# Optimization experiments

Hardware: AMD Instinct MI355X
Metric: run time of the kernel (lower is better)

The kernel has to match this reference:

```python
import jax, jax.numpy as jnp
import numpy as np

N = 100000   # total nodes in batched graph
E = 600000   # total edges
B = 64       # graphs in batch
H = 128      # hidden_dim
A = 64       # action_dim
L = 4        # num mpnn layers
LOG_STD_MIN, LOG_STD_MAX = -20.0, 2.0


def setup_inputs() -> dict:
    key = jax.random.key(0)
    ks = jax.random.split(key, 40)
    s = 0.05

    def w(k, shape):
        return (jax.random.normal(k, shape, jnp.float32) * s)

    inp = {}
    inp["node_feat"] = jax.random.normal(ks[0], (N, 7), jnp.float32)
    inp["edge_feat"] = jax.random.normal(ks[1], (E, 2), jnp.float32)
    # node encoder: Linear(7,H) -> ReLU -> Linear(H,H)
    inp["ne_w1"] = w(ks[2], (7, H)); inp["ne_b1"] = jnp.zeros((H,), jnp.float32)
    inp["ne_w2"] = w(ks[3], (H, H)); inp["ne_b2"] = jnp.zeros((H,), jnp.float32)
    # edge encoder: Linear(2,H) -> ReLU -> Linear(H,H)
    inp["ee_w1"] = w(ks[4], (2, H)); inp["ee_b1"] = jnp.zeros((H,), jnp.float32)
    inp["ee_w2"] = w(ks[5], (H, H)); inp["ee_b2"] = jnp.zeros((H,), jnp.float32)
    # per-layer message net: Linear(3H,H) -> ReLU -> Linear(H,H)  (stacked over L)
    inp["msg_w1"] = w(ks[6], (L, 3 * H, H)); inp["msg_b1"] = jnp.zeros((L, H), jnp.float32)
    inp["msg_w2"] = w(ks[7], (L, H, H));     inp["msg_b2"] = jnp.zeros((L, H), jnp.float32)
    # per-layer update net: Linear(2H,H) -> ReLU -> Linear(H,H)
    inp["upd_w1"] = w(ks[8], (L, 2 * H, H)); inp["upd_b1"] = jnp.zeros((L, H), jnp.float32)
    inp["upd_w2"] = w(ks[9], (L, H, H));     inp["upd_b2"] = jnp.zeros((L, H), jnp.float32)
    # attention-pooling gate: Linear(H,H) -> ReLU -> Linear(H,1)
    inp["gate_w1"] = w(ks[10], (H, H)); inp["gate_b1"] = jnp.zeros((H,), jnp.float32)
    inp["gate_w2"] = w(ks[11], (H, 1)); inp["gate_b2"] = jnp.zeros((1,), jnp.float32)
    # policy net: Linear(H,H) -> ReLU -> Linear(H,H) -> ReLU -> Linear(H,2A)
    inp["pol_w1"] = w(ks[12], (H, H));     inp["pol_b1"] = jnp.zeros((H,), jnp.float32)
    inp["pol_w2"] = w(ks[13], (H, H));     inp["pol_b2"] = jnp.zeros((H,), jnp.float32)
    inp["pol_w3"] = w(ks[14], (H, 2 * A)); inp["pol_b3"] = jnp.zeros((2 * A,), jnp.float32)
    # graph connectivity
    inp["src"] = jax.random.randint(ks[15], (E,), 0, N)
    inp["dst"] = jax.random.randint(ks[16], (E,), 0, N)
    inp["graph_id"] = jnp.sort(jax.random.randint(ks[17], (N,), 0, B))
    return inp


def _mlp2(x, w1, b1, w2, b2):
    return jax.nn.relu(x @ w1 + b1) @ w2 + b2


def reference(node_feat, edge_feat,
              ne_w1, ne_b1, ne_w2, ne_b2,
              ee_w1, ee_b1, ee_w2, ee_b2,
              msg_w1, msg_b1, msg_w2, msg_b2,
              upd_w1, upd_b1, upd_w2, upd_b2,
              gate_w1, gate_b1, gate_w2, gate_b2,
              pol_w1, pol_b1, pol_w2, pol_b2, pol_w3, pol_b3,
              src, dst, graph_id):
    # encode
    h = _mlp2(node_feat, ne_w1, ne_b1, ne_w2, ne_b2)          # [N, H]
    e = _mlp2(edge_feat, ee_w1, ee_b1, ee_w2, ee_b2)          # [E, H]
    # MPNN layers with residual (h = layer(h) + h)
    for l in range(L):
        msg_in = jnp.concatenate([h[src], h[dst], e], axis=1)  # [E, 3H]
        m = _mlp2(msg_in, msg_w1[l], msg_b1[l], msg_w2[l], msg_b2[l])  # [E, H]
        h_agg = jax.ops.segment_sum(m, dst, num_segments=N)    # [N, H]
        upd_in = jnp.concatenate([h, h_agg], axis=1)           # [N, 2H]
        h = _mlp2(upd_in, upd_w1[l], upd_b1[l], upd_w2[l], upd_b2[l]) + h
    # global attention pooling (per-graph segment softmax over gate logits)
    gate = _mlp2(h, gate_w1, gate_b1, gate_w2, gate_b2)[:, 0]  # [N]
    gmax = jax.ops.segment_max(gate, graph_id, num_segments=B)  # [B]
    ex = jnp.exp(gate - gmax[graph_id])                        # [N]
    z = jax.ops.segment_sum(ex, graph_id, num_segments=B)      # [B]
    alpha = ex / z[graph_id]                                   # [N]
    emb = jax.ops.segment_sum(alpha[:, None] * h, graph_id, num_segments=B)  # [B, H]
    # policy head
    out = jax.nn.relu(jax.nn.relu(emb @ pol_w1 + pol_b1) @ pol_w2 + pol_b2) @ pol_w3 + pol_b3  # [B, 2A]
    mean, log_std = out[:, :A], out[:, A:]
    log_std = jnp.clip(log_std, LOG_STD_MIN, LOG_STD_MAX)
    std = jnp.exp(log_std)
    return (mean, std)
```

## Files before the change

### kernel.cpp

```cpp
#include <hip/hip_runtime.h>
#include <stdint.h>

#define NN 100000
#define NE 600000
#define NG 64
#define HD 128
#define HD2 (HD*HD)
#define NLAYER 4
#define SCAN_NB 391
#define NTILES ((NN + 63) / 64)
#define PSLICE 16

typedef unsigned short u16;
typedef unsigned int u32;
typedef unsigned long long u64;
typedef __attribute__((ext_vector_type(8))) short bf16x8;
typedef __attribute__((ext_vector_type(4))) float f32x4;

__device__ __forceinline__ float bf2f(u32 v) { return __uint_as_float(v << 16); }
__device__ __forceinline__ u16 f2bf(float f) {
    u32 u = __float_as_uint(f);
    return (u16)((u + 0x7FFFu + ((u >> 16) & 1u)) >> 16);
}
__device__ __forceinline__ u32 pk2(float a, float b) {
    return (u32)f2bf(a) | ((u32)f2bf(b) << 16);
}

template<bool RELU, bool GATE>
__global__ __launch_bounds__(256, 3) void mgemm_kernel(
    const u16* __restrict__ Xb, const u16* __restrict__ Wt,
    const float* __restrict__ bias, const float* __restrict__ degscale,
    const u16* __restrict__ addend, u16* __restrict__ out, int M,
    const float* __restrict__ gw2, const float* __restrict__ gb2,
    float* __restrict__ gate)
{
    __shared__ u16 WsL[HD * HD];
    __shared__ u16 XsL[64 * HD];
    const int t = threadIdx.x;
    const int lane = t & 63, wave = t >> 6;
    const int cj = ((lane >> 4) << 2);

    for (int i = t; i < HD * 16; i += 256) {
        const int row = i >> 4, c16 = i & 15;
        uint4 v = *(const uint4*)(Wt + (size_t)row * HD + c16 * 8);
        *(uint4*)((char*)WsL + (((row << 8) + (c16 << 4)) ^ ((row & 7) << 4))) = v;
    }
    float4 bcol[8];
    #pragma unroll
    for (int ct = 0; ct < 8; ct++)
        bcol[ct] = bias ? *(const float4*)(bias + ct * 16 + cj)
                        : make_float4(0.f, 0.f, 0.f, 0.f);
    float4 gwv[8];
    if (GATE) {
        #pragma unroll
        for (int ct = 0; ct < 8; ct++)
            gwv[ct] = *(const float4*)(gw2 + ct * 16 + cj);
    }

    const int arow = wave * 16 + (lane & 15);
    const int alin = (arow << 8) + ((lane >> 4) << 4);
    const int axor = (arow & 7) << 4;
    __syncthreads();

    for (int tile = blockIdx.x; tile < NTILES; tile += gridDim.x) {
        const int r0 = tile << 6;
        for (int i = t; i < 64 * 16; i += 256) {
            const int row = i >> 4, c16 = i & 15;
            const int rg = r0 + row;
            uint4 v = make_uint4(0, 0, 0, 0);
            if (rg < M) v = *(const uint4*)(Xb + (size_t)rg * HD + c16 * 8);
            *(uint4*)((char*)XsL + (((row << 8) + (c16 << 4)) ^ ((row & 7) << 4))) = v;
        }
        __syncthreads();

        bf16x8 a[4];
        #pragma unroll
        for (int ks = 0; ks < 4; ks++)
            a[ks] = *(const bf16x8*)((const char*)XsL + ((alin + ks * 64) ^ axor));

        f32x4 acc[8];
        #pragma unroll
        for (int ct = 0; ct < 8; ct++) {
            acc[ct][0] = 0.f; acc[ct][1] = 0.f; acc[ct][2] = 0.f; acc[ct][3] = 0.f;
        }
        #pragma unroll
        for (int ct = 0; ct < 8; ct++) {
            const int bn = ct * 16 + (lane & 15);
            #pragma unroll
            for (int ks = 0; ks < 4; ks++) {
                bf16x8 breg = *(const bf16x8*)((const char*)WsL +
                    (((bn << 8) + ks * 64 + ((lane >> 4) << 4)) ^ ((bn & 7) << 4)));
                acc[ct] = __builtin_amdgcn_mfma_f32_16x16x32_bf16(breg, a[ks], acc[ct], 0, 0, 0);
            }
        }

        const int orow = r0 + wave * 16 + (lane & 15);
        const bool rv = orow < M;
        float gdot = 0.f;
        const float ds = (degscale && rv) ? degscale[orow] : 1.f;
        #pragma unroll
        for (int ct = 0; ct < 8; ct++) {
            const int c0 = ct * 16 + cj;
            float v0 = acc[ct][0], v1 = acc[ct][1], v2 = acc[ct][2], v3 = acc[ct][3];
            if (bias) {
                v0 += bcol[ct].x * ds; v1 += bcol[ct].y * ds;
                v2 += bcol[ct].z * ds; v3 += bcol[ct].w * ds;
            }
            if (addend && rv) {
                ushort4 av = *(const ushort4*)(addend + (size_t)orow * HD + c0);
                v0 += bf2f(av.x); v1 += bf2f(av.y); v2 += bf2f(av.z); v3 += bf2f(av.w);
            }
            if (RELU) {
                v0 = fmaxf(v0, 0.f); v1 = fmaxf(v1, 0.f);
                v2 = fmaxf(v2, 0.f); v3 = fmaxf(v3, 0.f);
            }
            if (GATE) {
                gdot += v0 * gwv[ct].x + v1 * gwv[ct].y + v2 * gwv[ct].z + v3 * gwv[ct].w;
            } else if (rv) {
                ushort4 pk;
                pk.x = f2bf(v0); pk.y = f2bf(v1); pk.z = f2bf(v2); pk.w = f2bf(v3);
                *(ushort4*)(out + (size_t)orow * HD + c0) = pk;
            }
        }
        if (GATE) {
            gdot += __shfl_xor(gdot, 16, 64);
            gdot += __shfl_xor(gdot, 32, 64);
            if ((lane >> 4) == 0 && rv) gate[orow] = gdot + gb2[0];
        }
        __syncthreads();
    }
}

__global__ __launch_bounds__(256, 2) void pqtgemm_kernel(
    const u16* __restrict__ Xb, const u16* __restrict__ WtP,
    const u16* __restrict__ WtQ, const u16* __restrict__ WtT,
    const float* __restrict__ tb, u16* __restrict__ outP,
    u16* __restrict__ outQ, u16* __restrict__ outT, int M)
{
    __shared__ u16 WsL[2 * HD * HD];
    __shared__ u16 XsL[64 * HD];
    const int t = threadIdx.x;
    const int lane = t & 63, wave = t >> 6;
    const int cj = ((lane >> 4) << 2);

    for (int i = t; i < 2 * HD * 16; i += 256) {
        const int w = i >> 11;
        const int j = i & 2047;
        const int row = j >> 4, c16 = j & 15;
        const u16* Wt = w ? WtQ : WtP;
        uint4 v = *(const uint4*)(Wt + (size_t)row * HD + c16 * 8);
        *(uint4*)((char*)WsL + w * 32768 +
                  (((row << 8) + (c16 << 4)) ^ ((row & 7) << 4))) = v;
    }
    bf16x8 treg[8][4];
    #pragma unroll
    for (int ct = 0; ct < 8; ct++) {
        const int bn = ct * 16 + (lane & 15);
        #pragma unroll
        for (int ks = 0; ks < 4; ks++)
            treg[ct][ks] = *(const bf16x8*)(WtT + (size_t)bn * HD + ks * 32 + ((lane >> 4) << 3));
    }
    float4 tbc[8];
    #pragma unroll
    for (int ct = 0; ct < 8; ct++)
        tbc[ct] = *(const float4*)(tb + ct * 16 + cj);

    const int arow = wave * 16 + (lane & 15);
    const int alin = (arow << 8) + ((lane >> 4) << 4);
    const int axor = (arow & 7) << 4;
    __syncthreads();

    for (int tile = blockIdx.x; tile < NTILES; tile += gridDim.x) {
        const int r0 = tile << 6;
        for (int i = t; i < 64 * 16; i += 256) {
            const int row = i >> 4, c16 = i & 15;
            const int rg = r0 + row;
            uint4 v = make_uint4(0, 0, 0, 0);
            if (rg < M) v = *(const uint4*)(Xb + (size_t)rg * HD + c16 * 8);
            *(uint4*)((char*)XsL + (((row << 8) + (c16 << 4)) ^ ((row & 7) << 4))) = v;
        }
        __syncthreads();

        bf16x8 a[4];
        #pragma unroll
        for (int ks = 0; ks < 4; ks++)
            a[ks] = *(const bf16x8*)((const char*)XsL + ((alin + ks * 64) ^ axor));

        const int orow = r0 + wave * 16 + (lane & 15);
        const bool rv = orow < M;

        #pragma unroll
        for (int o = 0; o < 2; o++) {
            f32x4 acc[8];
            #pragma unroll
            for (int ct = 0; ct < 8; ct++) {
                acc[ct][0] = 0.f; acc[ct][1] = 0.f; acc[ct][2] = 0.f; acc[ct][3] = 0.f;
            }
            #pragma unroll
            for (int ct = 0; ct < 8; ct++) {
                const int bn = ct * 16 + (lane & 15);
                #pragma unroll
                for (int ks = 0; ks < 4; ks++) {
                    bf16x8 breg = *(const bf16x8*)((const char*)WsL + o * 32768 +
                        (((bn << 8) + ks * 64 + ((lane >> 4) << 4)) ^ ((bn & 7) << 4)));
                    acc[ct] = __builtin_amdgcn_mfma_f32_16x16x32_bf16(breg, a[ks], acc[ct], 0, 0, 0);
                }
            }
            if (rv) {
                u16* out = o ? outQ : outP;
                #pragma unroll
                for (int ct = 0; ct < 8; ct++) {
                    ushort4 pk;
                    pk.x = f2bf(acc[ct][0]); pk.y = f2bf(acc[ct][1]);
                    pk.z = f2bf(acc[ct][2]); pk.w = f2bf(acc[ct][3]);
                    *(ushort4*)(out + (size_t)orow * HD + ct * 16 + cj) = pk;
                }
            }
        }
        {
            f32x4 acc[8];
            #pragma unroll
            for (int ct = 0; ct < 8; ct++) {
                acc[ct][0] = 0.f; acc[ct][1] = 0.f; acc[ct][2] = 0.f; acc[ct][3] = 0.f;
            }
            #pragma unroll
            for (int ct = 0; ct < 8; ct++)
                #pragma unroll
                for (int ks = 0; ks < 4; ks++)
                    acc[ct] = __builtin_amdgcn_mfma_f32_16x16x32_bf16(treg[ct][ks], a[ks], acc[ct], 0, 0, 0);
            if (rv) {
                #pragma unroll
                for (int ct = 0; ct < 8; ct++) {
                    ushort4 pk;
                    pk.x = f2bf(acc[ct][0] + tbc[ct].x);
                    pk.y = f2bf(acc[ct][1] + tbc[ct].y);
                    pk.z = f2bf(acc[ct][2] + tbc[ct].z);
                    pk.w = f2bf(acc[ct][3] + tbc[ct].w);
                    *(ushort4*)(outT + (size_t)orow * HD + ct * 16 + cj) = pk;
                }
            }
        }
        __syncthreads();
    }
}

__global__ __launch_bounds__(256, 2) void edge_mfma_kernel(
    const float2* __restrict__ sef, const int* __restrict__ ssrc,
    const int* __restrict__ sdst, const int* __restrict__ off,
    const float* __restrict__ ew1, const float* __restrict__ eb1,
    const u16* __restrict__ Mt, const float* __restrict__ mvec,
    const u16* __restrict__ P, const u16* __restrict__ Q,
    u16* __restrict__ agg)
{
    __shared__ __align__(16) char XHT[HD * 72 * 2];
    __shared__ u16 PsL[64 * 136];
    __shared__ u16 QsL[32 * 136];
    __shared__ u64 dlocL[8];
    __shared__ int nsrcL[2][64];
    __shared__ float ew1L[2 * HD];
    __shared__ float eb1L[HD];
    u16* HT = (u16*)XHT;
    const int t = threadIdx.x, lane = t & 63, wave = t >> 6;
    const int cj = (lane >> 4) << 2;
    const int n0 = blockIdx.x * 32;

    ew1L[t] = ew1[t];
    if (t < HD) eb1L[t] = eb1[t];
    for (int i = t; i < 32 * 32; i += 256) {
        const int row = i >> 5, c4 = (i & 31) * 4;
        *(ushort4*)(QsL + row * 136 + c4) = *(const ushort4*)(Q + (size_t)(n0 + row) * HD + c4);
    }

    float4 mvv[8];
    #pragma unroll
    for (int ct = 0; ct < 8; ct++) mvv[ct] = *(const float4*)(mvec + ct * 16 + cj);

    bf16x8 breg[8][4];
    #pragma unroll
    for (int ct = 0; ct < 8; ct++) {
        const int bn = ct * 16 + (lane & 15);
        #pragma unroll
        for (int ks = 0; ks < 4; ks++)
            breg[ct][ks] = *(const bf16x8*)(Mt + (size_t)bn * HD + ks * 32 + ((lane >> 4) << 3));
    }

    const int rt = wave & 1;
    const int c2b = (wave >> 1) * 4;
    const int nodeid = rt * 16 + (lane & 15);
    f32x4 acc2[4];
    #pragma unroll
    for (int i = 0; i < 4; i++) {
        acc2[i][0] = 0.f; acc2[i][1] = 0.f; acc2[i][2] = 0.f; acc2[i][3] = 0.f;
    }

    const int e0 = off[n0], e1 = off[n0 + 32];
    const int arow = wave * 16 + (lane & 15);
    const int alin = (arow << 8) + ((lane >> 4) << 4);
    const int axor = (arow & 7) << 4;
    const int el = wave * 16 + (lane & 15);
    if (t < 64) nsrcL[0][t] = (e0 + t < e1) ? ssrc[e0 + t] : 0;
    __syncthreads();

    int buf = 0;
    for (int base = e0; base < e1; base += 64) {
        for (int i = t; i < 64 * 16; i += 256) {
            const int row = i >> 4, c16 = i & 15;
            const int e = base + row;
            uint4 v = make_uint4(0, 0, 0, 0);
            uint4 pvv = make_uint4(0, 0, 0, 0);
            if (e < e1) {
                const float2 f = sef[e];
                const int c8 = c16 * 8;
                float o[8];
                #pragma unroll
                for (int k = 0; k < 8; k++)
                    o[k] = fmaxf(f.x * ew1L[c8 + k] + f.y * ew1L[HD + c8 + k] + eb1L[c8 + k], 0.f);
                v = make_uint4(pk2(o[0], o[1]), pk2(o[2], o[3]), pk2(o[4], o[5]), pk2(o[6], o[7]));
                const int srcI = nsrcL[buf][row];
                pvv = *(const uint4*)(P + (size_t)srcI * HD + c16 * 8);
            }
            *(uint4*)(XHT + (((row << 8) + (c16 << 4)) ^ ((row & 7) << 4))) = v;
            *(uint4*)(PsL + row * 136 + c16 * 8) = pvv;
        }
        if (t < 64) {
            const int e = base + t;
            ((unsigned char*)dlocL)[t] = (e < e1) ? (unsigned char)(sdst[e] - n0) : (unsigned char)0xFF;
            const int e2 = base + 64 + t;
            nsrcL[buf ^ 1][t] = (e2 < e1) ? ssrc[e2] : 0;
        }
        __syncthreads();

        bf16x8 a[4];
        #pragma unroll
        for (int ks = 0; ks < 4; ks++)
            a[ks] = *(const bf16x8*)(XHT + ((alin + ks * 64) ^ axor));
        const int e = base + el;
        const bool ev = e < e1;
        const int dl = ev ? (int)((const unsigned char*)dlocL)[el] : 0;
        __syncthreads();

        f32x4 acc[8];
        #pragma unroll
        for (int ct = 0; ct < 8; ct++) {
            acc[ct][0] = 0.f; acc[ct][1] = 0.f; acc[ct][2] = 0.f; acc[ct][3] = 0.f;
        }
        #pragma unroll
        for (int ct = 0; ct < 8; ct++)
            #pragma unroll
            for (int ks = 0; ks < 4; ks++)
                acc[ct] = __builtin_amdgcn_mfma_f32_16x16x32_bf16(breg[ct][ks], a[ks], acc[ct], 0, 0, 0);

        #pragma unroll
        for (int ct = 0; ct < 8; ct++) {
            float v0 = 0.f, v1 = 0.f, v2 = 0.f, v3 = 0.f;
            if (ev) {
                const ushort4 pvc = *(const ushort4*)(PsL + el * 136 + ct * 16 + cj);
                const ushort4 qvc = *(const ushort4*)(QsL + dl * 136 + ct * 16 + cj);
                v0 = fmaxf(acc[ct][0] + bf2f(pvc.x) + bf2f(qvc.x) + mvv[ct].x, 0.f);
                v1 = fmaxf(acc[ct][1] + bf2f(pvc.y) + bf2f(qvc.y) + mvv[ct].y, 0.f);
                v2 = fmaxf(acc[ct][2] + bf2f(pvc.z) + bf2f(qvc.z) + mvv[ct].z, 0.f);
                v3 = fmaxf(acc[ct][3] + bf2f(pvc.w) + bf2f(qvc.w) + mvv[ct].w, 0.f);
            }
            const int c0 = ct * 16 + cj;
            HT[(c0 + 0) * 72 + el] = f2bf(v0);
            HT[(c0 + 1) * 72 + el] = f2bf(v1);
            HT[(c0 + 2) * 72 + el] = f2bf(v2);
            HT[(c0 + 3) * 72 + el] = f2bf(v3);
        }
        __syncthreads();

        #pragma unroll
        for (int ks2 = 0; ks2 < 2; ks2++) {
            const u64 dv = dlocL[ks2 * 4 + (lane >> 4)];
            bf16x8 sfrag;
            #pragma unroll
            for (int j = 0; j < 8; j++) {
                const int dvj = (int)((dv >> (8 * j)) & 0xFF);
                sfrag[j] = (dvj == nodeid) ? (short)0x3F80 : (short)0;
            }
            #pragma unroll
            for (int i = 0; i < 4; i++) {
                const int col = (c2b + i) * 16 + (lane & 15);
                bf16x8 hfrag = *(const bf16x8*)(HT + col * 72 + ks2 * 32 + ((lane >> 4) << 3));
                acc2[i] = __builtin_amdgcn_mfma_f32_16x16x32_bf16(sfrag, hfrag, acc2[i], 0, 0, 0);
            }
        }
        __syncthreads();
        buf ^= 1;
    }

    u16* BNC = (u16*)XHT;
    #pragma unroll
    for (int i = 0; i < 4; i++) {
        const int col = (c2b + i) * 16 + (lane & 15);
        #pragma unroll
        for (int r = 0; r < 4; r++) {
            const int nl = rt * 16 + ((lane >> 4) << 2) + r;
            BNC[nl * 136 + col] = f2bf(acc2[i][r]);
        }
    }
    __syncthreads();
    for (int i = t; i < 32 * 16; i += 256) {
        const int row = i >> 4, c16 = i & 15;
        *(uint4*)(agg + (size_t)(n0 + row) * HD + c16 * 8) =
            *(const uint4*)(BNC + row * 136 + c16 * 8);
    }
}

__global__ __launch_bounds__(256) void foldgemm_kernel(
    const float* __restrict__ ee_w2, const float* __restrict__ msg_w1,
    const float* __restrict__ msg_w2, const float* __restrict__ upd_w1,
    float* __restrict__ Mw, float* __restrict__ Mw2)
{
    __shared__ float Ws[HD * HD];
    __shared__ float Xs[32 * HD];
    const int m = blockIdx.x >> 2;
    const int l = m & 3;
    const float* X; const float* W; float* outp;
    if (m < 4) {
        X = ee_w2;
        W = msg_w1 + (size_t)l * 3 * HD2 + 2 * HD2;
        outp = Mw + (size_t)l * HD2;
    } else {
        X = msg_w2 + (size_t)l * HD2;
        W = upd_w1 + (size_t)l * 2 * HD2 + HD2;
        outp = Mw2 + (size_t)l * HD2;
    }
    const int t = threadIdx.x;
    for (int i = t; i < HD2 / 4; i += 256)
        ((float4*)Ws)[i] = ((const float4*)W)[i];
    const int c0 = (t & 31) * 4;
    const int rb = (t >> 5) * 4;
    const int r0 = (blockIdx.x & 3) * 32;
    for (int i = t; i < 32 * HD / 4; i += 256)
        ((float4*)Xs)[i] = ((const float4*)(X + (size_t)r0 * HD))[i];
    __syncthreads();
    float acc[4][4];
    #pragma unroll
    for (int a = 0; a < 4; a++)
        #pragma unroll
        for (int b = 0; b < 4; b++) acc[a][b] = 0.f;
    for (int k = 0; k < HD; k += 4) {
        float4 w0 = *(const float4*)(Ws + (k + 0) * HD + c0);
        float4 w1 = *(const float4*)(Ws + (k + 1) * HD + c0);
        float4 w2 = *(const float4*)(Ws + (k + 2) * HD + c0);
        float4 w3 = *(const float4*)(Ws + (k + 3) * HD + c0);
        #pragma unroll
        for (int rr = 0; rr < 4; rr++) {
            float4 xv = *(const float4*)(Xs + (rb + rr) * HD + k);
            acc[rr][0] += xv.x * w0.x + xv.y * w1.x + xv.z * w2.x + xv.w * w3.x;
            acc[rr][1] += xv.x * w0.y + xv.y * w1.y + xv.z * w2.y + xv.w * w3.y;
            acc[rr][2] += xv.x * w0.z + xv.y * w1.z + xv.z * w2.z + xv.w * w3.z;
            acc[rr][3] += xv.x * w0.w + xv.y * w1.w + xv.z * w2.w + xv.w * w3.w;
        }
    }
    #pragma unroll
    for (int rr = 0; rr < 4; rr++) {
        const int row = r0 + rb + rr;
        *(float4*)(outp + (size_t)row * HD + c0) =
            make_float4(acc[rr][0], acc[rr][1], acc[rr][2], acc[rr][3]);
    }
}

__global__ void mvecb_kernel(
    const float* __restrict__ ee_b2, const float* __restrict__ msg_w1,
    const float* __restrict__ msg_b1, const float* __restrict__ msg_b2,
    const float* __restrict__ upd_w1, float* __restrict__ mvec,
    float* __restrict__ b2u)
{
    const int m = blockIdx.x;
    const int l = m & 3;
    const int j = threadIdx.x;
    if (j >= HD) return;
    if (m < 4) {
        const float* W = msg_w1 + (size_t)l * 3 * HD2 + 2 * HD2;
        float s = msg_b1[(size_t)l * HD + j];
        for (int i = 0; i < HD; i++) s += ee_b2[i] * W[(size_t)i * HD + j];
        mvec[(size_t)l * HD + j] = s;
    } else {
        const float* W = upd_w1 + (size_t)l * 2 * HD2 + HD2;
        float s = 0.f;
        for (int i = 0; i < HD; i++) s += msg_b2[(size_t)l * HD + i] * W[(size_t)i * HD + j];
        b2u[(size_t)l * HD + j] = s;
    }
}

__global__ __launch_bounds__(256) void wprep_kernel(
    const float* __restrict__ msg_w1, const float* __restrict__ Mw2,
    const float* __restrict__ upd_w1, const float* __restrict__ upd_w2,
    const float* __restrict__ gw1, const float* __restrict__ ne_w2,
    const float* __restrict__ Mw, u16* __restrict__ wt)
{
    __shared__ float tileL[HD * (HD + 1)];
    const int b = blockIdx.x, t = threadIdx.x;
    const int l = b & 3;
    const float* S;
    if (b < 4)       S = msg_w1 + (size_t)l * 3 * HD2;
    else if (b < 8)  S = msg_w1 + (size_t)l * 3 * HD2 + HD2;
    else if (b < 12) S = Mw + (size_t)l * HD2;
    else if (b < 16) S = Mw2 + (size_t)l * HD2;
    else if (b < 20) S = upd_w1 + (size_t)l * 2 * HD2;
    else if (b < 24) S = upd_w1 + (size_t)l * 2 * HD2 + HD2;
    else if (b < 28) S = upd_w2 + (size_t)l * HD2;
    else if (b == 28) S = gw1;
    else             S = ne_w2;
    u16* D = wt + (size_t)b * HD2;
    for (int i = t; i < HD2; i += 256) {
        const int k = i >> 7, n = i & 127;
        tileL[k * (HD + 1) + n] = S[i];
    }
    __syncthreads();
    for (int i = t; i < HD2; i += 256) {
        const int n = i >> 7, k = i & 127;
        D[i] = f2bf(tileL[k * (HD + 1) + n]);
    }
}

__global__ __launch_bounds__(256) void ne1_kernel(
    const float* __restrict__ nf, const float* __restrict__ w1,
    const float* __restrict__ b1, u16* __restrict__ out)
{
    __shared__ float w1s[7 * HD];
    __shared__ float b1s[HD];
    const int t = threadIdx.x;
    for (int i = t; i < 7 * HD; i += 256) w1s[i] = w1[i];
    if (t < HD) b1s[t] = b1[t];
    __syncthreads();
    const int row = blockIdx.x * 32 + (t >> 3);
    const int c0 = (t & 7) * 16;
    if (row < NN) {
        float f[7];
        #pragma unroll
        for (int k = 0; k < 7; k++) f[k] = nf[(size_t)row * 7 + k];
        float o[16];
        #pragma unroll
        for (int c = 0; c < 16; c++) {
            float a = b1s[c0 + c];
            #pragma unroll
            for (int k = 0; k < 7; k++) a += f[k] * w1s[k * HD + c0 + c];
            o[c] = fmaxf(a, 0.f);
        }
        uint4 v0 = make_uint4(pk2(o[0], o[1]), pk2(o[2], o[3]), pk2(o[4], o[5]), pk2(o[6], o[7]));
        uint4 v1 = make_uint4(pk2(o[8], o[9]), pk2(o[10], o[11]), pk2(o[12], o[13]), pk2(o[14], o[15]));
        *(uint4*)(out + (size_t)row * HD + c0) = v0;
        *(uint4*)(out + (size_t)row * HD + c0 + 8) = v1;
    }
}

__global__ void deg_count_kernel(const int* __restrict__ dst, int* __restrict__ deg) {
    const int i = blockIdx.x * 256 + threadIdx.x;
    if (i < NE) atomicAdd(&deg[dst[i]], 1);
}
__global__ void scan1_kernel(const int* __restrict__ deg, int* __restrict__ part) {
    __shared__ int s[256];
    const int t = threadIdx.x, i = blockIdx.x * 256 + t;
    s[t] = (i < NN) ? deg[i] : 0;
    __syncthreads();
    for (int d = 128; d > 0; d >>= 1) { if (t < d) s[t] += s[t + d]; __syncthreads(); }
    if (t == 0) part[blockIdx.x] = s[0];
}
__global__ void scan2_kernel(int* __restrict__ part, int nb) {
    if (threadIdx.x == 0 && blockIdx.x == 0) {
        int run = 0;
        for (int b = 0; b < nb; b++) { const int v = part[b]; part[b] = run; run += v; }
    }
}
__global__ void scan3_kernel(const int* __restrict__ deg, const int* __restrict__ part,
                             int* __restrict__ off, int* __restrict__ pos,
                             float* __restrict__ degf) {
    __shared__ int s[256];
    const int t = threadIdx.x, i = blockIdx.x * 256 + t;
    const int v = (i < NN) ? deg[i] : 0;
    s[t] = v;
    __syncthreads();
    for (int d = 1; d < 256; d <<= 1) {
        const int x = (t >= d) ? s[t - d] : 0;
        __syncthreads();
        s[t] += x;
        __syncthreads();
    }
    const int excl = s[t] - v + part[blockIdx.x];
    if (i < NN) {
        off[i] = excl; pos[i] = excl;
        degf[i] = (float)v;
        if (i == NN - 1) off[NN] = excl + v;
    }
}
__global__ void scatter_kernel(const int* __restrict__ src, const int* __restrict__ dst,
                               const float* __restrict__ ef, int* __restrict__ pos,
                               float2* __restrict__ sef, int* __restrict__ ssrc,
                               int* __restrict__ sdst) {
    const int e = blockIdx.x * 256 + threadIdx.x;
    if (e < NE) {
        const int d = dst[e];
        const int p = atomicAdd(&pos[d], 1);
        sef[p] = make_float2(ef[2 * e], ef[2 * e + 1]);
        ssrc[p] = src[e]; sdst[p] = d;
    }
}

__global__ void bounds_kernel(const int* __restrict__ gid, int* __restrict__ gs) {
    const int g = threadIdx.x;
    if (g <= NG) {
        int lo = 0, hi = NN;
        while (lo < hi) {
            const int mid = (lo + hi) >> 1;
            if (gid[mid] < g) lo = mid + 1; else hi = mid;
        }
        gs[g] = lo;
    }
}

__global__ __launch_bounds__(256) void poolA_kernel(
    const float* __restrict__ gate, const int* __restrict__ gs,
    float* __restrict__ ex, float* __restrict__ gz)
{
    __shared__ float red[256];
    const int g = blockIdx.x, t = threadIdx.x;
    const int s = gs[g], e = gs[g + 1];
    if (s >= e) {
        if (t == 0) gz[g] = 1.f;
        return;
    }
    float m = -3.4e38f;
    for (int i = s + t; i < e; i += 256) m = fmaxf(m, gate[i]);
    red[t] = m; __syncthreads();
    for (int d = 128; d > 0; d >>= 1) {
        if (t < d) red[t] = fmaxf(red[t], red[t + d]);
        __syncthreads();
    }
    const float gm = red[0];
    __syncthreads();
    float zs = 0.f;
    for (int i = s + t; i < e; i += 256) {
        const float ev = expf(gate[i] - gm);
        ex[i] = ev; zs += ev;
    }
    red[t] = zs; __syncthreads();
    for (int d = 128; d > 0; d >>= 1) {
        if (t < d) red[t] += red[t + d];
        __syncthreads();
    }
    if (t == 0) gz[g] = red[0];
}

__global__ __launch_bounds__(256) void poolB_kernel(
    const float* __restrict__ ex, const int* __restrict__ gs,
    const u16* __restrict__ hb, float* __restrict__ partial)
{
    __shared__ float redL[16][132];
    const int b = blockIdx.x;
    const int g = b / PSLICE, sl = b % PSLICE;
    const int lo = gs[g], hi = gs[g + 1];
    const int len = hi - lo;
    const int chunk = (len + PSLICE - 1) / PSLICE;
    const int ns = lo + sl * chunk;
    const int ne = min(ns + chunk, hi);
    const int t = threadIdx.x;
    const int c8 = (t & 15) * 8;
    const int ro = t >> 4;
    float acc[8] = {0.f, 0.f, 0.f, 0.f, 0.f, 0.f, 0.f, 0.f};
    for (int n = ns + ro; n < ne; n += 16) {
        const float w = ex[n];
        const ushort4 h0 = *(const ushort4*)(hb + (size_t)n * HD + c8);
        const ushort4 h1 = *(const ushort4*)(hb + (size_t)n * HD + c8 + 4);
        acc[0] += w * bf2f(h0.x); acc[1] += w * bf2f(h0.y);
        acc[2] += w * bf2f(h0.z); acc[3] += w * bf2f(h0.w);
        acc[4] += w * bf2f(h1.x); acc[5] += w * bf2f(h1.y);
        acc[6] += w * bf2f(h1.z); acc[7] += w * bf2f(h1.w);
    }
    #pragma unroll
    for (int j = 0; j < 8; j++) redL[ro][c8 + j] = acc[j];
    __syncthreads();
    if (t < HD) {
        float s = 0.f;
        #pragma unroll
        for (int r = 0; r < 16; r++) s += redL[r][t];
        partial[(size_t)b * HD + t] = s;
    }
}

__global__ void poolC_kernel(const float* __restrict__ partial,
                             const float* __restrict__ gz,
                             float* __restrict__ emb)
{
    const int g = blockIdx.x, t = threadIdx.x;
    float s = 0.f;
    #pragma unroll
    for (int sl = 0; sl < PSLICE; sl++)
        s += partial[(size_t)(g * PSLICE + sl) * HD + t];
    emb[(size_t)g * HD + t] = s / gz[g];
}

__global__ __launch_bounds__(256) void policy_kernel(
    const float* __restrict__ emb,
    const float* __restrict__ w1, const float* __restrict__ b1,
    const float* __restrict__ w2, const float* __restrict__ b2,
    const float* __restrict__ w3, const float* __restrict__ b3,
    float* __restrict__ out)
{
    __shared__ float A[NG * HD];
    __shared__ float Bs[NG * HD];
    const int t = threadIdx.x;
    for (int i = t; i < NG * HD / 4; i += 256)
        ((float4*)A)[i] = ((const float4*)emb)[i];
    __syncthreads();
    const int c0 = (t & 31) * 4;
    const int rb = (t >> 5) * 8;
    {
        float4 bv = *(const float4*)(b1 + c0);
        for (int rr = 0; rr < 8; rr++) {
            const int r = rb + rr;
            float a0 = bv.x, a1 = bv.y, a2 = bv.z, a3 = bv.w;
            for (int k = 0; k < HD; k++) {
                const float x = A[r * HD + k];
                float4 wv = *(const float4*)(w1 + k * HD + c0);
                a0 += x * wv.x; a1 += x * wv.y; a2 += x * wv.z; a3 += x * wv.w;
            }
            *(float4*)(Bs + r * HD + c0) =
                make_float4(fmaxf(a0, 0.f), fmaxf(a1, 0.f), fmaxf(a2, 0.f), fmaxf(a3, 0.f));
        }
    }
    __syncthreads();
    {
        float4 bv = *(const float4*)(b2 + c0);
        for (int rr = 0; rr < 8; rr++) {
            const int r = rb + rr;
            float a0 = bv.x, a1 = bv.y, a2 = bv.z, a3 = bv.w;
            for (int k = 0; k < HD; k++) {
                const float x = Bs[r * HD + k];
                float4 wv = *(const float4*)(w2 + k * HD + c0);
                a0 += x * wv.x; a1 += x * wv.y; a2 += x * wv.z; a3 += x * wv.w;
            }
            *(float4*)(A + r * HD + c0) =
                make_float4(fmaxf(a0, 0.f), fmaxf(a1, 0.f), fmaxf(a2, 0.f), fmaxf(a3, 0.f));
        }
    }
    __syncthreads();
    {
        float4 bv = *(const float4*)(b3 + c0);
        for (int rr = 0; rr < 8; rr++) {
            const int r = rb + rr;
            float a[4] = {bv.x, bv.y, bv.z, bv.w};
            for (int k = 0; k < HD; k++) {
                const float x = A[r * HD + k];
                float4 wv = *(const float4*)(w3 + k * HD + c0);
                a[0] += x * wv.x; a[1] += x * wv.y; a[2] += x * wv.z; a[3] += x * wv.w;
            }
            #pragma unroll
            for (int j = 0; j < 4; j++) {
                const int c = c0 + j;
                if (c < 64) {
                    out[r * 64 + c] = a[j];
                } else {
                    const float ls = fminf(fmaxf(a[j], -20.f), 2.f);
                    out[4096 + r * 64 + (c - 64)] = expf(ls);
                }
            }
        }
    }
}

extern "C" void kernel_launch(void* const* d_in, const int* in_sizes, int n_in,
                              void* d_out, int out_size, void* d_ws, size_t ws_size,
                              hipStream_t stream) {
    const float* node_feat = (const float*)d_in[0];
    const float* edge_feat = (const float*)d_in[1];
    const float* ne_w1 = (const float*)d_in[2];
    const float* ne_b1 = (const float*)d_in[3];
    const float* ne_w2 = (const float*)d_in[4];
    const float* ne_b2 = (const float*)d_in[5];
    const float* ee_w1 = (const float*)d_in[6];
    const float* ee_b1 = (const float*)d_in[7];
    const float* ee_w2 = (const float*)d_in[8];
    const float* ee_b2 = (const float*)d_in[9];
    const float* msg_w1 = (const float*)d_in[10];
    const float* msg_b1 = (const float*)d_in[11];
    const float* msg_w2 = (const float*)d_in[12];
    const float* msg_b2 = (const float*)d_in[13];
    const float* upd_w1 = (const float*)d_in[14];
    const float* upd_b1 = (const float*)d_in[15];
    const float* upd_w2 = (const float*)d_in[16];
    const float* upd_b2 = (const float*)d_in[17];
    const float* gate_w1 = (const float*)d_in[18];
    const float* gate_b1 = (const float*)d_in[19];
    const float* gate_w2 = (const float*)d_in[20];
    const float* gate_b2 = (const float*)d_in[21];
    const float* pol_w1 = (const float*)d_in[22];
    const float* pol_b1 = (const float*)d_in[23];
    const float* pol_w2 = (const float*)d_in[24];
    const float* pol_b2 = (const float*)d_in[25];
    const float* pol_w3 = (const float*)d_in[26];
    const float* pol_b3 = (const float*)d_in[27];
    const int* src = (const int*)d_in[28];
    const int* dst = (const int*)d_in[29];
    const int* gid = (const int*)d_in[30];

    char* p = (char*)d_ws;
    u16* hb   = (u16*)p;    p += (size_t)NN * HD * 2;
    u16* Pb   = (u16*)p;    p += (size_t)NN * HD * 2;
    u16* Qb   = (u16*)p;    p += (size_t)NN * HD * 2;
    u16* aggb = (u16*)p;    p += (size_t)NN * HD * 2;
    u16* tub  = (u16*)p;    p += (size_t)NN * HD * 2;
    float2* sef = (float2*)p; p += (size_t)NE * 8;
    int* ssrc = (int*)p;    p += (size_t)NE * 4;
    int* sdst = (int*)p;    p += (size_t)NE * 4;
    int* off  = (int*)p;    p += (size_t)(NN + 4) * 4;
    int* pos  = (int*)p;    p += (size_t)NN * 4;
    int* deg  = (int*)p;    p += (size_t)NN * 4;
    float* degf = (float*)p; p += (size_t)NN * 4;
    float* gate = (float*)p; p += (size_t)NN * 4;
    float* ex   = (float*)p; p += (size_t)NN * 4;
    int* part = (int*)p;    p += 2048;
    int* gs   = (int*)p;    p += 512;
    float* gz   = (float*)p; p += 256;
    float* emb = (float*)p; p += (size_t)NG * HD * 4;
    float* partialP = (float*)p; p += (size_t)NG * PSLICE * HD * 4;
    float* Mw  = (float*)p; p += (size_t)NLAYER * HD2 * 4;
    float* Mw2 = (float*)p; p += (size_t)NLAYER * HD2 * 4;
    float* mvec = (float*)p; p += (size_t)NLAYER * HD * 4;
    float* b2u  = (float*)p; p += (size_t)NLAYER * HD * 4;
    u16* wt = (u16*)p;      p += (size_t)30 * HD2 * 2;

    hipMemsetAsync(deg, 0, (size_t)NN * 4, stream);
    deg_count_kernel<<<(NE + 255) / 256, 256, 0, stream>>>(dst, deg);
    scan1_kernel<<<SCAN_NB, 256, 0, stream>>>(deg, part);
    scan2_kernel<<<1, 64, 0, stream>>>(part, SCAN_NB);
    scan3_kernel<<<SCAN_NB, 256, 0, stream>>>(deg, part, off, pos, degf);
    scatter_kernel<<<(NE + 255) / 256, 256, 0, stream>>>(src, dst, edge_feat, pos, sef, ssrc, sdst);
    bounds_kernel<<<1, 128, 0, stream>>>(gid, gs);

    foldgemm_kernel<<<32, 256, 0, stream>>>(ee_w2, msg_w1, msg_w2, upd_w1, Mw, Mw2);
    mvecb_kernel<<<8, 128, 0, stream>>>(ee_b2, msg_w1, msg_b1, msg_b2, upd_w1, mvec, b2u);
    wprep_kernel<<<30, 256, 0, stream>>>(msg_w1, Mw2, upd_w1, upd_w2, gate_w1, ne_w2, Mw, wt);

    ne1_kernel<<<3125, 256, 0, stream>>>(node_feat, ne_w1, ne_b1, Pb);
    mgemm_kernel<false, false><<<512, 256, 0, stream>>>(
        Pb, wt + (size_t)29 * HD2, ne_b2, nullptr, nullptr, hb, NN, nullptr, nullptr, nullptr);

    for (int l = 0; l < NLAYER; l++) {
        pqtgemm_kernel<<<512, 256, 0, stream>>>(
            hb, wt + (size_t)(0 + l) * HD2, wt + (size_t)(4 + l) * HD2,
            wt + (size_t)(16 + l) * HD2, upd_b1 + (size_t)l * HD, Pb, Qb, tub, NN);
        edge_mfma_kernel<<<NN / 32, 256, 0, stream>>>(sef, ssrc, sdst, off, ee_w1, ee_b1,
            wt + (size_t)(8 + l) * HD2, mvec + (size_t)l * HD, Pb, Qb, aggb);
        mgemm_kernel<true, false><<<512, 256, 0, stream>>>(
            aggb, wt + (size_t)(12 + l) * HD2, b2u + (size_t)l * HD, degf, tub, Pb, NN,
            nullptr, nullptr, nullptr);
        mgemm_kernel<false, false><<<512, 256, 0, stream>>>(
            Pb, wt + (size_t)(24 + l) * HD2, upd_b2 + (size_t)l * HD, nullptr, hb, hb, NN,
            nullptr, nullptr, nullptr);
    }

    mgemm_kernel<true, true><<<512, 256, 0, stream>>>(
        hb, wt + (size_t)28 * HD2, gate_b1, nullptr, nullptr, nullptr, NN,
        gate_w2, gate_b2, gate);
    poolA_kernel<<<NG, 256, 0, stream>>>(gate, gs, ex, gz);
    poolB_kernel<<<NG * PSLICE, 256, 0, stream>>>(ex, gs, hb, partialP);
    poolC_kernel<<<NG, 128, 0, stream>>>(partialP, gz, emb);
    policy_kernel<<<1, 256, 0, stream>>>(emb, pol_w1, pol_b1, pol_w2, pol_b2, pol_w3, pol_b3, (float*)d_out);
}
```

Measured before the change: 1.306 ms.

## Fuse two update-MLP GEMMs per layer into one kernel keeping intermediate in LDS

Adds an updgemm kernel that runs the first update GEMM (agg times folded weights, plus degree-scaled bias, precomputed term and ReLU) and stores its bf16 result in shared memory. The second GEMM with residual add then runs in the same kernel, so the intermediate never goes through global memory and one launch per layer disappears. The first weight matrix is staged in LDS and the second is held in registers, which raises LDS and register pressure. Grid size for the remaining standalone mgemm launches also goes from 512 to 768 blocks.

```diff
diff --git a/kernel.cpp b/kernel.cpp
--- a/kernel.cpp
+++ b/kernel.cpp
@@ -237,6 +237,131 @@
                     pk.z = f2bf(acc[ct][2] + tbc[ct].z);
                     pk.w = f2bf(acc[ct][3] + tbc[ct].w);
                     *(ushort4*)(outT + (size_t)orow * HD + ct * 16 + cj) = pk;
+                }
+            }
+        }
+        __syncthreads();
+    }
+}
+
+__global__ __launch_bounds__(256, 2) void updgemm_kernel(
+    const u16* __restrict__ aggb, const u16* __restrict__ WtA,
+    const u16* __restrict__ WtB, const float* __restrict__ b2u,
+    const float* __restrict__ degf, const u16* __restrict__ tub,
+    const float* __restrict__ ub2, u16* __restrict__ hb, int M)
+{
+    __shared__ u16 WsL[HD * HD];
+    __shared__ u16 XsL[64 * HD];
+    __shared__ u16 HsL[64 * HD];
+    const int t = threadIdx.x;
+    const int lane = t & 63, wave = t >> 6;
+    const int cj = ((lane >> 4) << 2);
+
+    for (int i = t; i < HD * 16; i += 256) {
+        const int row = i >> 4, c16 = i & 15;
+        uint4 v = *(const uint4*)(WtA + (size_t)row * HD + c16 * 8);
+        *(uint4*)((char*)WsL + (((row << 8) + (c16 << 4)) ^ ((row & 7) << 4))) = v;
+    }
+    bf16x8 treg[8][4];
+    #pragma unroll
+    for (int ct = 0; ct < 8; ct++) {
+        const int bn = ct * 16 + (lane & 15);
+        #pragma unroll
+        for (int ks = 0; ks < 4; ks++)
+            treg[ct][ks] = *(const bf16x8*)(WtB + (size_t)bn * HD + ks * 32 + ((lane >> 4) << 3));
+    }
+    float4 b1c[8], b2c[8];
+    #pragma unroll
+    for (int ct = 0; ct < 8; ct++) {
+        b1c[ct] = *(const float4*)(b2u + ct * 16 + cj);
+        b2c[ct] = *(const float4*)(ub2 + ct * 16 + cj);
+    }
+
+    const int arow = wave * 16 + (lane & 15);
+    const int alin = (arow << 8) + ((lane >> 4) << 4);
+    const int axor = (arow & 7) << 4;
+    __syncthreads();
+
+    for (int tile = blockIdx.x; tile < NTILES; tile += gridDim.x) {
+        const int r0 = tile << 6;
+        for (int i = t; i < 64 * 16; i += 256) {
+            const int row = i >> 4, c16 = i & 15;
+            const int rg = r0 + row;
+            uint4 v = make_uint4(0, 0, 0, 0);
+            if (rg < M) v = *(const uint4*)(aggb + (size_t)rg * HD + c16 * 8);
+            *(uint4*)((char*)XsL + (((row << 8) + (c16 << 4)) ^ ((row & 7) << 4))) = v;
+        }
+        __syncthreads();
+
+        const int orow = r0 + wave * 16 + (lane & 15);
+        const bool rv = orow < M;
+        {
+            bf16x8 a[4];
+            #pragma unroll
+            for (int ks = 0; ks < 4; ks++)
+                a[ks] = *(const bf16x8*)((const char*)XsL + ((alin + ks * 64) ^ axor));
+            f32x4 acc[8];
+            #pragma unroll
+            for (int ct = 0; ct < 8; ct++) {
+                acc[ct][0] = 0.f; acc[ct][1] = 0.f; acc[ct][2] = 0.f; acc[ct][3] = 0.f;
+            }
+            #pragma unroll
+            for (int ct = 0; ct < 8; ct++) {
+                const int bn = ct * 16 + (lane & 15);
+                #pragma unroll
+                for (int ks = 0; ks < 4; ks++) {
+                    bf16x8 breg = *(const bf16x8*)((const char*)WsL +
+                        (((bn << 8) + ks * 64 + ((lane >> 4) << 4)) ^ ((bn & 7) << 4)));
+                    acc[ct] = __builtin_amdgcn_mfma_f32_16x16x32_bf16(breg, a[ks], acc[ct], 0, 0, 0);
+                }
+            }
+            const float ds = rv ? degf[orow] : 0.f;
+            const int lrow = wave * 16 + (lane & 15);
+            #pragma unroll
+            for (int ct = 0; ct < 8; ct++) {
+                const int c0 = ct * 16 + cj;
+                float v0 = acc[ct][0] + b1c[ct].x * ds;
+                float v1 = acc[ct][1] + b1c[ct].y * ds;
+                float v2 = acc[ct][2] + b1c[ct].z * ds;
+                float v3 = acc[ct][3] + b1c[ct].w * ds;
+                if (rv) {
+                    ushort4 tv = *(const ushort4*)(tub + (size_t)orow * HD + c0);
+                    v0 += bf2f(tv.x); v1 += bf2f(tv.y); v2 += bf2f(tv.z); v3 += bf2f(tv.w);
+                }
+                v0 = fmaxf(v0, 0.f); v1 = fmaxf(v1, 0.f);
+                v2 = fmaxf(v2, 0.f); v3 = fmaxf(v3, 0.f);
+                ushort4 pk;
+                pk.x = f2bf(v0); pk.y = f2bf(v1); pk.z = f2bf(v2); pk.w = f2bf(v3);
+                *(ushort4*)((char*)HsL + (((lrow << 8) + c0 * 2) ^ ((lrow & 7) << 4))) = pk;
+            }
+        }
+        __syncthreads();
+        {
+            bf16x8 a[4];
+            #pragma unroll
+            for (int ks = 0; ks < 4; ks++)
+                a[ks] = *(const bf16x8*)((const char*)HsL + ((alin + ks * 64) ^ axor));
+            f32x4 acc[8];
+            #pragma unroll
+            for (int ct = 0; ct < 8; ct++) {
+                acc[ct][0] = 0.f; acc[ct][1] = 0.f; acc[ct][2] = 0.f; acc[ct][3] = 0.f;
+            }
+            #pragma unroll
+            for (int ct = 0; ct < 8; ct++)
+                #pragma unroll
+                for (int ks = 0; ks < 4; ks++)
+                    acc[ct] = __builtin_amdgcn_mfma_f32_16x16x32_bf16(treg[ct][ks], a[ks], acc[ct], 0, 0, 0);
+            if (rv) {
+                #pragma unroll
+                for (int ct = 0; ct < 8; ct++) {
+                    const int c0 = ct * 16 + cj;
+                    ushort4 hv = *(const ushort4*)(hb + (size_t)orow * HD + c0);
+                    ushort4 pk;
+                    pk.x = f2bf(acc[ct][0] + b2c[ct].x + bf2f(hv.x));
+                    pk.y = f2bf(acc[ct][1] + b2c[ct].y + bf2f(hv.y));
+                    pk.z = f2bf(acc[ct][2] + b2c[ct].z + bf2f(hv.z));
+                    pk.w = f2bf(acc[ct][3] + b2c[ct].w + bf2f(hv.w));
+                    *(ushort4*)(hb + (size_t)orow * HD + c0) = pk;
                 }
             }
         }
@@ -835,7 +960,7 @@
     wprep_kernel<<<30, 256, 0, stream>>>(msg_w1, Mw2, upd_w1, upd_w2, gate_w1, ne_w2, Mw, wt);
 
     ne1_kernel<<<3125, 256, 0, stream>>>(node_feat, ne_w1, ne_b1, Pb);
-    mgemm_kernel<false, false><<<512, 256, 0, stream>>>(
+    mgemm_kernel<false, false><<<768, 256, 0, stream>>>(
         Pb, wt + (size_t)29 * HD2, ne_b2, nullptr, nullptr, hb, NN, nullptr, nullptr, nullptr);
 
     for (int l = 0; l < NLAYER; l++) {
@@ -844,15 +969,12 @@
             wt + (size_t)(16 + l) * HD2, upd_b1 + (size_t)l * HD, Pb, Qb, tub, NN);
         edge_mfma_kernel<<<NN / 32, 256, 0, stream>>>(sef, ssrc, sdst, off, ee_w1, ee_b1,
             wt + (size_t)(8 + l) * HD2, mvec + (size_t)l * HD, Pb, Qb, aggb);
-        mgemm_kernel<true, false><<<512, 256, 0, stream>>>(
-            aggb, wt + (size_t)(12 + l) * HD2, b2u + (size_t)l * HD, degf, tub, Pb, NN,
-            nullptr, nullptr, nullptr);
-        mgemm_kernel<false, false><<<512, 256, 0, stream>>>(
-            Pb, wt + (size_t)(24 + l) * HD2, upd_b2 + (size_t)l * HD, nullptr, hb, hb, NN,
-            nullptr, nullptr, nullptr);
-    }
-
-    mgemm_kernel<true, true><<<512, 256, 0, stream>>>(
+        updgemm_kernel<<<512, 256, 0, stream>>>(
+            aggb, wt + (size_t)(12 + l) * HD2, wt + (size_t)(24 + l) * HD2,
+            b2u + (size_t)l * HD, degf, tub, upd_b2 + (size_t)l * HD, hb, NN);
+    }
+
+    mgemm_kernel<true, true><<<768, 256, 0, stream>>>(
         hb, wt + (size_t)28 * HD2, gate_b1, nullptr, nullptr, nullptr, NN,
         gate_w2, gate_b2, gate);
     poolA_kernel<<<NG, 256, 0, stream>>>(gate, gs, ex, gz);
```

New measurement: 1.316 ms. About the same (+0.7%).
